# Performance work log

Hardware: AMD Instinct MI355X
Metric: run time of the kernel (lower is better)

The kernel has to match this reference:

```python
import jax, jax.numpy as jnp
import numpy as np

TEMPERATURE = 0.1
EPS_NORM = 1e-12   # F.normalize eps
EPS_DEN = 1e-08


def setup_inputs() -> dict:
    key = jax.random.key(0)
    k1, k2 = jax.random.split(key)
    N, D = 8192, 256
    representations = jax.random.normal(k1, (N, D), dtype=jnp.float32)
    pseudo_labels = jax.random.randint(k2, (N,), 0, 100, dtype=jnp.int64)
    return {"representations": representations, "pseudo_labels": pseudo_labels}


def reference(representations, pseudo_labels):
    N = representations.shape[0]
    # L2 normalize rows (torch F.normalize semantics: x / max(||x||, eps))
    norm = jnp.linalg.norm(representations, axis=1, keepdims=True)
    r = representations / jnp.maximum(norm, EPS_NORM)
    # N x N cosine similarity
    sim = r @ r.T
    same = pseudo_labels[:, None] == pseudo_labels[None, :]
    eye = jnp.eye(N, dtype=bool)
    positive_mask = (same & ~eye).astype(sim.dtype)   # diag removed
    negative_mask = (~same).astype(sim.dtype)
    numerator = jnp.exp(sim * positive_mask / TEMPERATURE)
    num_diag = jnp.diagonal(numerator)                 # = exp(0) = 1 on diag
    denominator = jnp.sum(jnp.exp(sim * negative_mask / TEMPERATURE), axis=1) + num_diag
    loss = jnp.mean(-jnp.log(num_diag / (denominator + EPS_DEN)))
    return loss
```

## Files before the change

kernel.cpp:

```cpp
#include <hip/hip_runtime.h>
#include <hip/hip_bf16.h>
#include <hip/hip_fp8.h>
#include <stdint.h>

typedef __attribute__((ext_vector_type(4))) float f32x4;
typedef __attribute__((ext_vector_type(4))) unsigned int u32x4;
typedef __attribute__((ext_vector_type(8))) int i32x8;

#define N_ROWS 8192
#define DIM 256
#define BM 128
#define BJ 128
#define JCHUNKS 8
#define JCHUNK (N_ROWS / JCHUNKS)

#define SCL 3.79828252f

#define UNIT_SCALE 0x7F7F7F7F

__global__ void k_norm(const float* __restrict__ reps,
                       unsigned char* __restrict__ rq,
                       float* __restrict__ den,
                       float* __restrict__ out) {
  const int w = threadIdx.x >> 6, lane = threadIdx.x & 63;
  const int row = blockIdx.x * 4 + w;
  const float4 v = reinterpret_cast<const float4*>(reps + row * DIM)[lane];
  float ss = v.x * v.x + v.y * v.y + v.z * v.z + v.w * v.w;
#pragma unroll
  for (int m = 1; m < 64; m <<= 1) ss += __shfl_xor(ss, m);
  const float scale = SCL / fmaxf(sqrtf(ss), 1e-12f);
  const uint32_t b0 = __hip_fp8_e4m3(v.x * scale).__x;
  const uint32_t b1 = __hip_fp8_e4m3(v.y * scale).__x;
  const uint32_t b2 = __hip_fp8_e4m3(v.z * scale).__x;
  const uint32_t b3 = __hip_fp8_e4m3(v.w * scale).__x;
  *reinterpret_cast<uint32_t*>(rq + (size_t)row * DIM + lane * 4) =
      b0 | (b1 << 8) | (b2 << 16) | (b3 << 24);
  if (threadIdx.x < 4) den[blockIdx.x * 4 + threadIdx.x] = 0.0f;
  if (blockIdx.x == 0 && threadIdx.x == 0) out[0] = 0.0f;
}

__global__ __launch_bounds__(256, 2) void k_sim(
    const unsigned char* __restrict__ rq,
    const int* __restrict__ lab,
    float* __restrict__ den) {
  __shared__ unsigned char Bs[2][BJ * DIM];

  const int tid = threadIdx.x;
  const int w = tid >> 6, lane = tid & 63;
  const int l15 = lane & 15, lq = lane >> 4;
  const int ibase = blockIdx.x * BM + w * 32;
  const int jc0 = blockIdx.y * JCHUNK;

  i32x8 a[2][2];
#pragma unroll
  for (int t = 0; t < 2; ++t) {
    const unsigned char* ap = rq + (size_t)(ibase + t * 16 + l15) * DIM + lq * 32;
#pragma unroll
    for (int kc = 0; kc < 2; ++kc) {
      const u32x4 v0 = *reinterpret_cast<const u32x4*>(ap + kc * 128);
      const u32x4 v1 = *reinterpret_cast<const u32x4*>(ap + kc * 128 + 16);
      a[t][kc] = (i32x8){(int)v0.x, (int)v0.y, (int)v0.z, (int)v0.w,
                         (int)v1.x, (int)v1.y, (int)v1.z, (int)v1.w};
    }
  }
  int labi[2][4];
#pragma unroll
  for (int t = 0; t < 2; ++t)
#pragma unroll
    for (int r = 0; r < 4; ++r)
      labi[t][r] = lab[ibase + t * 16 + lq * 4 + r];

  f32x4 dsum[2] = {{0.f, 0.f, 0.f, 0.f}, {0.f, 0.f, 0.f, 0.f}};

  const int lrow0 = w * 32;

#pragma unroll
  for (int q = 0; q < 8; ++q) {
    const int lrow = lrow0 + q * 4 + lq;
    const int ch = l15 ^ (lrow & 7);
    const unsigned char* g = rq + (size_t)(jc0 + lrow) * DIM + ch * 16;
    unsigned char* l = Bs[0] + (lrow0 + q * 4) * DIM;
    __builtin_amdgcn_global_load_lds(
        (const __attribute__((address_space(1))) uint32_t*)g,
        (__attribute__((address_space(3))) uint32_t*)l, 16, 0, 0);
  }

  for (int jt = 0; jt < JCHUNK / BJ; ++jt) {
    const int cur = jt & 1;
    const int j0 = jc0 + jt * BJ;

    __syncthreads();

    if (jt < JCHUNK / BJ - 1) {
      const int jn = j0 + BJ;
#pragma unroll
      for (int q = 0; q < 8; ++q) {
        const int lrow = lrow0 + q * 4 + lq;
        const int ch = l15 ^ (lrow & 7);
        const unsigned char* g = rq + (size_t)(jn + lrow) * DIM + ch * 16;
        unsigned char* l = Bs[cur ^ 1] + (lrow0 + q * 4) * DIM;
        __builtin_amdgcn_global_load_lds(
            (const __attribute__((address_space(1))) uint32_t*)g,
            (__attribute__((address_space(3))) uint32_t*)l, 16, 0, 0);
      }
    }

    int labj[8];
#pragma unroll
    for (int s = 0; s < 8; ++s) labj[s] = lab[j0 + s * 16 + l15];

    const unsigned char* Bb = Bs[cur];
#pragma unroll
    for (int s = 0; s < 8; ++s) {
      f32x4 acc0 = {0.f, 0.f, 0.f, 0.f};
      f32x4 acc1 = {0.f, 0.f, 0.f, 0.f};
      const int brow = s * 16 + l15;
      const unsigned char* bp = Bb + brow * DIM;
      const int sw = brow & 7;
#pragma unroll
      for (int kc = 0; kc < 2; ++kc) {
        const int base = kc * 8 + lq * 2;
        const u32x4 b0 = *reinterpret_cast<const u32x4*>(bp + (base ^ sw) * 16);
        const u32x4 b1 = *reinterpret_cast<const u32x4*>(bp + ((base + 1) ^ sw) * 16);
        const i32x8 bb = (i32x8){(int)b0.x, (int)b0.y, (int)b0.z, (int)b0.w,
                                 (int)b1.x, (int)b1.y, (int)b1.z, (int)b1.w};
        acc0 = __builtin_amdgcn_mfma_scale_f32_16x16x128_f8f6f4(
            a[0][kc], bb, acc0, 0, 0, 0, UNIT_SCALE, 0, UNIT_SCALE);
        acc1 = __builtin_amdgcn_mfma_scale_f32_16x16x128_f8f6f4(
            a[1][kc], bb, acc1, 0, 0, 0, UNIT_SCALE, 0, UNIT_SCALE);
      }
#pragma unroll
      for (int r = 0; r < 4; ++r) {
        float e0 = __builtin_amdgcn_exp2f(acc0[r]);
        float e1 = __builtin_amdgcn_exp2f(acc1[r]);
        dsum[0][r] += (labi[0][r] == labj[s]) ? 1.0f : e0;
        dsum[1][r] += (labi[1][r] == labj[s]) ? 1.0f : e1;
      }
    }
  }

#pragma unroll
  for (int t = 0; t < 2; ++t)
#pragma unroll
    for (int r = 0; r < 4; ++r) {
      float v = dsum[t][r];
      v += __shfl_xor(v, 1);
      v += __shfl_xor(v, 2);
      v += __shfl_xor(v, 4);
      v += __shfl_xor(v, 8);
      if (l15 == 0) atomicAdd(&den[ibase + t * 16 + lq * 4 + r], v);
    }
}

__global__ void k_loss(const float* __restrict__ den, float* __restrict__ out) {
  const int idx = blockIdx.x * 256 + threadIdx.x;
  float v = logf(den[idx] + 1.0f + 1e-8f);
#pragma unroll
  for (int m = 1; m < 64; m <<= 1) v += __shfl_xor(v, m);
  __shared__ float sred[4];
  if ((threadIdx.x & 63) == 0) sred[threadIdx.x >> 6] = v;
  __syncthreads();
  if (threadIdx.x == 0)
    atomicAdd(out, (sred[0] + sred[1] + sred[2] + sred[3]) * (1.0f / (float)N_ROWS));
}

extern "C" void kernel_launch(void* const* d_in, const int* in_sizes, int n_in,
                              void* d_out, int out_size, void* d_ws, size_t ws_size,
                              hipStream_t stream) {
  const float* reps = (const float*)d_in[0];
  const int* lab = (const int*)d_in[1];
  float* out = (float*)d_out;
  unsigned char* rq = (unsigned char*)d_ws;
  float* den = (float*)((char*)d_ws + (size_t)N_ROWS * DIM);

  k_norm<<<N_ROWS / 4, 256, 0, stream>>>(reps, rq, den, out);
  k_sim<<<dim3(N_ROWS / BM, JCHUNKS), 256, 0, stream>>>(rq, lab, den);
  k_loss<<<N_ROWS / 256, 256, 0, stream>>>(den, out);
}
```

Measured before the change: 35.35 us.

## Switch similarity tile to 32x32x64 FP8 MFMA with 256-row blocks

Replaces the 16x16x128 scaled FP8 MFMA with the 32x32x64 variant, so each wave computes a 64-row by 32-column tile per step. The block's row tile doubles to 256 and the column split doubles to 16 chunks. Labels are packed into bytes to keep register use down with the larger accumulators. This aims for higher MFMA throughput and more B-tile reuse from LDS, at the cost of more accumulator and exp work per thread and the loss of the occupancy hint.

Result: slower. 52.04 us (+47.2%).

```diff
diff --git a/kernel.cpp b/kernel.cpp
--- a/kernel.cpp
+++ b/kernel.cpp
@@ -4,14 +4,15 @@
 #include <stdint.h>
 
 typedef __attribute__((ext_vector_type(4))) float f32x4;
+typedef __attribute__((ext_vector_type(16))) float f32x16;
 typedef __attribute__((ext_vector_type(4))) unsigned int u32x4;
 typedef __attribute__((ext_vector_type(8))) int i32x8;
 
 #define N_ROWS 8192
 #define DIM 256
-#define BM 128
+#define BM 256
 #define BJ 128
-#define JCHUNKS 8
+#define JCHUNKS 16
 #define JCHUNK (N_ROWS / JCHUNKS)
 
 #define SCL 3.79828252f
@@ -39,7 +40,7 @@
   if (blockIdx.x == 0 && threadIdx.x == 0) out[0] = 0.0f;
 }
 
-__global__ __launch_bounds__(256, 2) void k_sim(
+__global__ __attribute__((amdgpu_flat_work_group_size(256, 256))) void k_sim(
     const unsigned char* __restrict__ rq,
     const int* __restrict__ lab,
     float* __restrict__ den) {
@@ -48,29 +49,40 @@
   const int tid = threadIdx.x;
   const int w = tid >> 6, lane = tid & 63;
   const int l15 = lane & 15, lq = lane >> 4;
-  const int ibase = blockIdx.x * BM + w * 32;
+  const int l31 = lane & 31, lh = lane >> 5;
+  const int ibase = blockIdx.x * BM + w * 64;
   const int jc0 = blockIdx.y * JCHUNK;
 
-  i32x8 a[2][2];
+  i32x8 a[2][4];
 #pragma unroll
   for (int t = 0; t < 2; ++t) {
-    const unsigned char* ap = rq + (size_t)(ibase + t * 16 + l15) * DIM + lq * 32;
+    const unsigned char* ap = rq + (size_t)(ibase + t * 32 + l31) * DIM + lh * 32;
 #pragma unroll
-    for (int kc = 0; kc < 2; ++kc) {
-      const u32x4 v0 = *reinterpret_cast<const u32x4*>(ap + kc * 128);
-      const u32x4 v1 = *reinterpret_cast<const u32x4*>(ap + kc * 128 + 16);
+    for (int kc = 0; kc < 4; ++kc) {
+      const u32x4 v0 = *reinterpret_cast<const u32x4*>(ap + kc * 64);
+      const u32x4 v1 = *reinterpret_cast<const u32x4*>(ap + kc * 64 + 16);
       a[t][kc] = (i32x8){(int)v0.x, (int)v0.y, (int)v0.z, (int)v0.w,
                          (int)v1.x, (int)v1.y, (int)v1.z, (int)v1.w};
     }
   }
-  int labi[2][4];
+
+  uint32_t labi_pk[2][4];
 #pragma unroll
   for (int t = 0; t < 2; ++t)
 #pragma unroll
-    for (int r = 0; r < 4; ++r)
-      labi[t][r] = lab[ibase + t * 16 + lq * 4 + r];
+    for (int g = 0; g < 4; ++g) {
+      const int base = ibase + t * 32 + 8 * g + 4 * lh;
+      labi_pk[t][g] = (uint32_t)(lab[base] & 0xFF) |
+                      ((uint32_t)(lab[base + 1] & 0xFF) << 8) |
+                      ((uint32_t)(lab[base + 2] & 0xFF) << 16) |
+                      ((uint32_t)(lab[base + 3] & 0xFF) << 24);
+    }
 
-  f32x4 dsum[2] = {{0.f, 0.f, 0.f, 0.f}, {0.f, 0.f, 0.f, 0.f}};
+  f32x16 dsum[2];
+#pragma unroll
+  for (int t = 0; t < 2; ++t)
+#pragma unroll
+    for (int r = 0; r < 16; ++r) dsum[t][r] = 0.0f;
 
   const int lrow0 = w * 32;
 
@@ -105,36 +117,42 @@
       }
     }
 
-    int labj[8];
-#pragma unroll
-    for (int s = 0; s < 8; ++s) labj[s] = lab[j0 + s * 16 + l15];
+    const uint32_t labj_pk =
+        (uint32_t)(lab[j0 + l31] & 0xFF) |
+        ((uint32_t)(lab[j0 + 32 + l31] & 0xFF) << 8) |
+        ((uint32_t)(lab[j0 + 64 + l31] & 0xFF) << 16) |
+        ((uint32_t)(lab[j0 + 96 + l31] & 0xFF) << 24);
 
     const unsigned char* Bb = Bs[cur];
 #pragma unroll
-    for (int s = 0; s < 8; ++s) {
-      f32x4 acc0 = {0.f, 0.f, 0.f, 0.f};
-      f32x4 acc1 = {0.f, 0.f, 0.f, 0.f};
-      const int brow = s * 16 + l15;
+    for (int s = 0; s < 4; ++s) {
+      f32x16 acc0, acc1;
+#pragma unroll
+      for (int r = 0; r < 16; ++r) { acc0[r] = 0.0f; acc1[r] = 0.0f; }
+      const int brow = s * 32 + l31;
       const unsigned char* bp = Bb + brow * DIM;
       const int sw = brow & 7;
 #pragma unroll
-      for (int kc = 0; kc < 2; ++kc) {
-        const int base = kc * 8 + lq * 2;
-        const u32x4 b0 = *reinterpret_cast<const u32x4*>(bp + (base ^ sw) * 16);
-        const u32x4 b1 = *reinterpret_cast<const u32x4*>(bp + ((base + 1) ^ sw) * 16);
+      for (int kc = 0; kc < 4; ++kc) {
+        const int c0 = kc * 4 + lh * 2;
+        const u32x4 b0 = *reinterpret_cast<const u32x4*>(bp + (c0 ^ sw) * 16);
+        const u32x4 b1 = *reinterpret_cast<const u32x4*>(bp + ((c0 + 1) ^ sw) * 16);
         const i32x8 bb = (i32x8){(int)b0.x, (int)b0.y, (int)b0.z, (int)b0.w,
                                  (int)b1.x, (int)b1.y, (int)b1.z, (int)b1.w};
-        acc0 = __builtin_amdgcn_mfma_scale_f32_16x16x128_f8f6f4(
+        acc0 = __builtin_amdgcn_mfma_scale_f32_32x32x64_f8f6f4(
             a[0][kc], bb, acc0, 0, 0, 0, UNIT_SCALE, 0, UNIT_SCALE);
-        acc1 = __builtin_amdgcn_mfma_scale_f32_16x16x128_f8f6f4(
+        acc1 = __builtin_amdgcn_mfma_scale_f32_32x32x64_f8f6f4(
             a[1][kc], bb, acc1, 0, 0, 0, UNIT_SCALE, 0, UNIT_SCALE);
       }
+      const int lj = (int)((labj_pk >> (s * 8)) & 0xFF);
 #pragma unroll
-      for (int r = 0; r < 4; ++r) {
-        float e0 = __builtin_amdgcn_exp2f(acc0[r]);
-        float e1 = __builtin_amdgcn_exp2f(acc1[r]);
-        dsum[0][r] += (labi[0][r] == labj[s]) ? 1.0f : e0;
-        dsum[1][r] += (labi[1][r] == labj[s]) ? 1.0f : e1;
+      for (int r = 0; r < 16; ++r) {
+        const float e0 = __builtin_amdgcn_exp2f(acc0[r]);
+        const float e1 = __builtin_amdgcn_exp2f(acc1[r]);
+        const int li0 = (int)((labi_pk[0][r >> 2] >> ((r & 3) * 8)) & 0xFF);
+        const int li1 = (int)((labi_pk[1][r >> 2] >> ((r & 3) * 8)) & 0xFF);
+        dsum[0][r] += (li0 == lj) ? 1.0f : e0;
+        dsum[1][r] += (li1 == lj) ? 1.0f : e1;
       }
     }
   }
@@ -142,13 +160,15 @@
 #pragma unroll
   for (int t = 0; t < 2; ++t)
 #pragma unroll
-    for (int r = 0; r < 4; ++r) {
+    for (int r = 0; r < 16; ++r) {
       float v = dsum[t][r];
       v += __shfl_xor(v, 1);
       v += __shfl_xor(v, 2);
       v += __shfl_xor(v, 4);
       v += __shfl_xor(v, 8);
-      if (l15 == 0) atomicAdd(&den[ibase + t * 16 + lq * 4 + r], v);
+      v += __shfl_xor(v, 16);
+      if (l31 == 0)
+        atomicAdd(&den[ibase + t * 32 + (r & 3) + 8 * (r >> 2) + 4 * lh], v);
     }
 }
 
```

## Exploit similarity symmetry by computing only lower-triangular tiles with column partial sums

Applied to the files above, without the earlier changes.

Each block now processes a balanced set of lower-triangular 128x128 tiles, paired as row p with row 63-p, instead of the full NxN grid. Off-diagonal tiles also produce column sums, which go through shared memory into a per-tile-row partial buffer, so the mirrored tile never has to be computed. The loss kernel then reduces 64 partials per row before the log. This roughly halves the MFMA and exp work. In exchange it adds a per-column cross-wave reduction, extra global writes and reads of an N x 64 partial array, and reloads of the A fragment when a block switches tile rows.

After: 52.01 us. +47.1%, slower.

```diff
diff --git a/kernel.cpp b/kernel.cpp
--- a/kernel.cpp
+++ b/kernel.cpp
@@ -4,23 +4,22 @@
 #include <stdint.h>
 
 typedef __attribute__((ext_vector_type(4))) float f32x4;
+typedef __attribute__((ext_vector_type(2))) unsigned int u32x2;
 typedef __attribute__((ext_vector_type(4))) unsigned int u32x4;
 typedef __attribute__((ext_vector_type(8))) int i32x8;
 
 #define N_ROWS 8192
 #define DIM 256
-#define BM 128
 #define BJ 128
-#define JCHUNKS 8
-#define JCHUNK (N_ROWS / JCHUNKS)
+#define NTILE 64
 
 #define SCL 3.79828252f
-
 #define UNIT_SCALE 0x7F7F7F7F
 
 __global__ void k_norm(const float* __restrict__ reps,
                        unsigned char* __restrict__ rq,
                        float* __restrict__ den,
+                       float* __restrict__ part,
                        float* __restrict__ out) {
   const int w = threadIdx.x >> 6, lane = threadIdx.x & 63;
   const int row = blockIdx.x * 4 + w;
@@ -35,80 +34,121 @@
   const uint32_t b3 = __hip_fp8_e4m3(v.w * scale).__x;
   *reinterpret_cast<uint32_t*>(rq + (size_t)row * DIM + lane * 4) =
       b0 | (b1 << 8) | (b2 << 16) | (b3 << 24);
+  part[blockIdx.x * 256 + threadIdx.x] = 0.0f;
   if (threadIdx.x < 4) den[blockIdx.x * 4 + threadIdx.x] = 0.0f;
   if (blockIdx.x == 0 && threadIdx.x == 0) out[0] = 0.0f;
 }
 
-__global__ __launch_bounds__(256, 2) void k_sim(
+__global__ __launch_bounds__(256, 2) void k_simt(
     const unsigned char* __restrict__ rq,
     const int* __restrict__ lab,
-    float* __restrict__ den) {
+    float* __restrict__ den,
+    float* __restrict__ part) {
   __shared__ unsigned char Bs[2][BJ * DIM];
+  __shared__ float colacc[2][4][128];
+
+  const int p = blockIdx.x >> 4;
+  const int q = blockIdx.x & 15;
+  const int c0 = q * 4 + (q > 0 ? 1 : 0);
+  const int nc = (q == 0) ? 5 : 4;
 
   const int tid = threadIdx.x;
   const int w = tid >> 6, lane = tid & 63;
   const int l15 = lane & 15, lq = lane >> 4;
-  const int ibase = blockIdx.x * BM + w * 32;
-  const int jc0 = blockIdx.y * JCHUNK;
+  const int lrow0 = w * 32;
+
+  {
+    int cc = c0;
+    const int tj = (cc <= p) ? cc : (cc - p - 1);
+#pragma unroll
+    for (int qq = 0; qq < 8; ++qq) {
+      const int lrow = lrow0 + qq * 4 + lq;
+      const int ch = l15 ^ (lrow & 7);
+      const unsigned char* g = rq + (size_t)(tj * 128 + lrow) * DIM + ch * 16;
+      unsigned char* l = Bs[0] + (lrow0 + qq * 4) * DIM;
+      __builtin_amdgcn_global_load_lds(
+          (const __attribute__((address_space(1))) uint32_t*)g,
+          (__attribute__((address_space(3))) uint32_t*)l, 16, 0, 0);
+    }
+  }
 
   i32x8 a[2][2];
-#pragma unroll
-  for (int t = 0; t < 2; ++t) {
-    const unsigned char* ap = rq + (size_t)(ibase + t * 16 + l15) * DIM + lq * 32;
-#pragma unroll
-    for (int kc = 0; kc < 2; ++kc) {
-      const u32x4 v0 = *reinterpret_cast<const u32x4*>(ap + kc * 128);
-      const u32x4 v1 = *reinterpret_cast<const u32x4*>(ap + kc * 128 + 16);
-      a[t][kc] = (i32x8){(int)v0.x, (int)v0.y, (int)v0.z, (int)v0.w,
-                         (int)v1.x, (int)v1.y, (int)v1.z, (int)v1.w};
-    }
-  }
   int labi[2][4];
-#pragma unroll
-  for (int t = 0; t < 2; ++t)
-#pragma unroll
-    for (int r = 0; r < 4; ++r)
-      labi[t][r] = lab[ibase + t * 16 + lq * 4 + r];
-
   f32x4 dsum[2] = {{0.f, 0.f, 0.f, 0.f}, {0.f, 0.f, 0.f, 0.f}};
-
-  const int lrow0 = w * 32;
-
-#pragma unroll
-  for (int q = 0; q < 8; ++q) {
-    const int lrow = lrow0 + q * 4 + lq;
-    const int ch = l15 ^ (lrow & 7);
-    const unsigned char* g = rq + (size_t)(jc0 + lrow) * DIM + ch * 16;
-    unsigned char* l = Bs[0] + (lrow0 + q * 4) * DIM;
-    __builtin_amdgcn_global_load_lds(
-        (const __attribute__((address_space(1))) uint32_t*)g,
-        (__attribute__((address_space(3))) uint32_t*)l, 16, 0, 0);
-  }
-
-  for (int jt = 0; jt < JCHUNK / BJ; ++jt) {
-    const int cur = jt & 1;
-    const int j0 = jc0 + jt * BJ;
+  int cur_ti = -1, cur_ibase = 0;
+  int prev_store = 0, prev_ti = 0, prev_tj = 0;
+
+  for (int idx = 0; idx < nc; ++idx) {
+    const int cc = c0 + idx;
+    const int cur = idx & 1;
+    int ti, tj;
+    if (cc <= p) { ti = p; tj = cc; }
+    else         { ti = 63 - p; tj = cc - p - 1; }
+    const int jbase = tj * 128;
 
     __syncthreads();
 
-    if (jt < JCHUNK / BJ - 1) {
-      const int jn = j0 + BJ;
-#pragma unroll
-      for (int q = 0; q < 8; ++q) {
-        const int lrow = lrow0 + q * 4 + lq;
+    if (idx + 1 < nc) {
+      const int ccn = cc + 1;
+      const int tjn = (ccn <= p) ? ccn : (ccn - p - 1);
+#pragma unroll
+      for (int qq = 0; qq < 8; ++qq) {
+        const int lrow = lrow0 + qq * 4 + lq;
         const int ch = l15 ^ (lrow & 7);
-        const unsigned char* g = rq + (size_t)(jn + lrow) * DIM + ch * 16;
-        unsigned char* l = Bs[cur ^ 1] + (lrow0 + q * 4) * DIM;
+        const unsigned char* g = rq + (size_t)(tjn * 128 + lrow) * DIM + ch * 16;
+        unsigned char* l = Bs[cur ^ 1] + (lrow0 + qq * 4) * DIM;
         __builtin_amdgcn_global_load_lds(
             (const __attribute__((address_space(1))) uint32_t*)g,
             (__attribute__((address_space(3))) uint32_t*)l, 16, 0, 0);
       }
     }
 
+    if (prev_store && tid < 128)
+      part[(size_t)prev_ti * N_ROWS + prev_tj * 128 + tid] =
+          colacc[cur ^ 1][0][tid] + colacc[cur ^ 1][1][tid] +
+          colacc[cur ^ 1][2][tid] + colacc[cur ^ 1][3][tid];
+
+    if (ti != cur_ti) {
+      if (cur_ti >= 0) {
+#pragma unroll
+        for (int t = 0; t < 2; ++t)
+#pragma unroll
+          for (int r = 0; r < 4; ++r) {
+            float v = dsum[t][r];
+            v += __shfl_xor(v, 1);
+            v += __shfl_xor(v, 2);
+            v += __shfl_xor(v, 4);
+            v += __shfl_xor(v, 8);
+            if (l15 == 0) atomicAdd(&den[cur_ibase + t * 16 + lq * 4 + r], v);
+            dsum[t][r] = 0.f;
+          }
+      }
+      cur_ti = ti;
+      cur_ibase = ti * 128 + w * 32;
+#pragma unroll
+      for (int t = 0; t < 2; ++t) {
+        const unsigned char* ap =
+            rq + (size_t)(cur_ibase + t * 16 + l15) * DIM + lq * 32;
+#pragma unroll
+        for (int kc = 0; kc < 2; ++kc) {
+          const u32x4 v0 = *reinterpret_cast<const u32x4*>(ap + kc * 128);
+          const u32x4 v1 = *reinterpret_cast<const u32x4*>(ap + kc * 128 + 16);
+          a[t][kc] = (i32x8){(int)v0.x, (int)v0.y, (int)v0.z, (int)v0.w,
+                             (int)v1.x, (int)v1.y, (int)v1.z, (int)v1.w};
+        }
+      }
+#pragma unroll
+      for (int t = 0; t < 2; ++t)
+#pragma unroll
+        for (int r = 0; r < 4; ++r)
+          labi[t][r] = lab[cur_ibase + t * 16 + lq * 4 + r];
+    }
+
     int labj[8];
 #pragma unroll
-    for (int s = 0; s < 8; ++s) labj[s] = lab[j0 + s * 16 + l15];
-
+    for (int s = 0; s < 8; ++s) labj[s] = lab[jbase + s * 16 + l15];
+
+    const bool offd = (ti != tj);
     const unsigned char* Bb = Bs[cur];
 #pragma unroll
     for (int s = 0; s < 8; ++s) {
@@ -129,16 +169,35 @@
         acc1 = __builtin_amdgcn_mfma_scale_f32_16x16x128_f8f6f4(
             a[1][kc], bb, acc1, 0, 0, 0, UNIT_SCALE, 0, UNIT_SCALE);
       }
+      float colp = 0.f;
 #pragma unroll
       for (int r = 0; r < 4; ++r) {
-        float e0 = __builtin_amdgcn_exp2f(acc0[r]);
-        float e1 = __builtin_amdgcn_exp2f(acc1[r]);
-        dsum[0][r] += (labi[0][r] == labj[s]) ? 1.0f : e0;
-        dsum[1][r] += (labi[1][r] == labj[s]) ? 1.0f : e1;
-      }
-    }
+        const float e0 = __builtin_amdgcn_exp2f(acc0[r]);
+        const float e1 = __builtin_amdgcn_exp2f(acc1[r]);
+        const float m0 = (labi[0][r] == labj[s]) ? 1.0f : e0;
+        const float m1 = (labi[1][r] == labj[s]) ? 1.0f : e1;
+        dsum[0][r] += m0;
+        dsum[1][r] += m1;
+        colp += m0 + m1;
+      }
+      if (offd) {
+        colp += __shfl_xor(colp, 16);
+        colp += __shfl_xor(colp, 32);
+        if (lane < 16) colacc[cur][w][s * 16 + l15] = colp;
+      }
+    }
+    prev_store = offd ? 1 : 0;
+    prev_ti = ti;
+    prev_tj = tj;
   }
 
+  __syncthreads();
+  if (prev_store && tid < 128) {
+    const int lastbuf = (nc - 1) & 1;
+    part[(size_t)prev_ti * N_ROWS + prev_tj * 128 + tid] =
+        colacc[lastbuf][0][tid] + colacc[lastbuf][1][tid] +
+        colacc[lastbuf][2][tid] + colacc[lastbuf][3][tid];
+  }
 #pragma unroll
   for (int t = 0; t < 2; ++t)
 #pragma unroll
@@ -148,13 +207,18 @@
       v += __shfl_xor(v, 2);
       v += __shfl_xor(v, 4);
       v += __shfl_xor(v, 8);
-      if (l15 == 0) atomicAdd(&den[ibase + t * 16 + lq * 4 + r], v);
-    }
-}
-
-__global__ void k_loss(const float* __restrict__ den, float* __restrict__ out) {
+      if (l15 == 0) atomicAdd(&den[cur_ibase + t * 16 + lq * 4 + r], v);
+    }
+}
+
+__global__ void k_loss(const float* __restrict__ den,
+                       const float* __restrict__ part,
+                       float* __restrict__ out) {
   const int idx = blockIdx.x * 256 + threadIdx.x;
-  float v = logf(den[idx] + 1.0f + 1e-8f);
+  float v = den[idx] + 1.0f + 1e-8f;
+#pragma unroll
+  for (int a2 = 0; a2 < NTILE; ++a2) v += part[(size_t)a2 * N_ROWS + idx];
+  v = logf(v);
 #pragma unroll
   for (int m = 1; m < 64; m <<= 1) v += __shfl_xor(v, m);
   __shared__ float sred[4];
@@ -172,8 +236,10 @@
   float* out = (float*)d_out;
   unsigned char* rq = (unsigned char*)d_ws;
   float* den = (float*)((char*)d_ws + (size_t)N_ROWS * DIM);
-
-  k_norm<<<N_ROWS / 4, 256, 0, stream>>>(reps, rq, den, out);
-  k_sim<<<dim3(N_ROWS / BM, JCHUNKS), 256, 0, stream>>>(rq, lab, den);
-  k_loss<<<N_ROWS / 256, 256, 0, stream>>>(den, out);
-}
+  float* part = (float*)((char*)d_ws + (size_t)N_ROWS * DIM
+                         + (size_t)N_ROWS * 4);
+
+  k_norm<<<N_ROWS / 4, 256, 0, stream>>>(reps, rq, den, part, out);
+  k_simt<<<512, 256, 0, stream>>>(rq, lab, den, part);
+  k_loss<<<N_ROWS / 256, 256, 0, stream>>>(den, part, out);
+}
```

## Quantize normalized rows to FP4 e2m1 and use scaled FP4 MFMA

Applied to the files above, without the earlier changes.

Normalized representations are now quantized to 4-bit e2m1 with a custom rounding function instead of fp8 e4m3, halving the stored row size. The similarity kernel loads half as many bytes into LDS and from global memory, and runs the scaled MFMA in fp4 mode with a block scale of 2^-3 to undo the pre-scaling. This cuts memory traffic and may raise MFMA throughput. The cost is a large loss of precision in the cosine similarities, which, after the divide by temperature and the exp, could move the loss far from the fp32 reference.

Result: faster. 30.28 us (-14.4%).

```diff
diff --git a/kernel.cpp b/kernel.cpp
--- a/kernel.cpp
+++ b/kernel.cpp
@@ -1,6 +1,5 @@
 #include <hip/hip_runtime.h>
 #include <hip/hip_bf16.h>
-#include <hip/hip_fp8.h>
 #include <stdint.h>
 
 typedef __attribute__((ext_vector_type(4))) float f32x4;
@@ -9,6 +8,7 @@
 
 #define N_ROWS 8192
 #define DIM 256
+#define ROWB 128
 #define BM 128
 #define BJ 128
 #define JCHUNKS 8
@@ -16,7 +16,16 @@
 
 #define SCL 3.79828252f
 
-#define UNIT_SCALE 0x7F7F7F7F
+#define SCALE_M3 0x7C7C7C7C
+
+__device__ __forceinline__ uint32_t q_e2m1(float y) {
+  const uint32_t s = (__builtin_bit_cast(uint32_t, y) >> 31) << 3;
+  const float a = fabsf(y);
+  const uint32_t c = (a < 0.25f) ? 0u : (a < 0.75f) ? 1u : (a < 1.25f) ? 2u
+                   : (a < 1.75f) ? 3u : (a < 2.5f)  ? 4u : (a < 3.5f)  ? 5u
+                   : (a < 5.0f)  ? 6u : 7u;
+  return s | c;
+}
 
 __global__ void k_norm(const float* __restrict__ reps,
                        unsigned char* __restrict__ rq,
@@ -28,13 +37,11 @@
   float ss = v.x * v.x + v.y * v.y + v.z * v.z + v.w * v.w;
 #pragma unroll
   for (int m = 1; m < 64; m <<= 1) ss += __shfl_xor(ss, m);
-  const float scale = SCL / fmaxf(sqrtf(ss), 1e-12f);
-  const uint32_t b0 = __hip_fp8_e4m3(v.x * scale).__x;
-  const uint32_t b1 = __hip_fp8_e4m3(v.y * scale).__x;
-  const uint32_t b2 = __hip_fp8_e4m3(v.z * scale).__x;
-  const uint32_t b3 = __hip_fp8_e4m3(v.w * scale).__x;
-  *reinterpret_cast<uint32_t*>(rq + (size_t)row * DIM + lane * 4) =
-      b0 | (b1 << 8) | (b2 << 16) | (b3 << 24);
+  const float qs = 8.0f * SCL / fmaxf(sqrtf(ss), 1e-12f);
+  const uint32_t nib = q_e2m1(v.x * qs) | (q_e2m1(v.y * qs) << 4) |
+                       (q_e2m1(v.z * qs) << 8) | (q_e2m1(v.w * qs) << 12);
+  *reinterpret_cast<unsigned short*>(rq + (size_t)row * ROWB + lane * 2) =
+      (unsigned short)nib;
   if (threadIdx.x < 4) den[blockIdx.x * 4 + threadIdx.x] = 0.0f;
   if (blockIdx.x == 0 && threadIdx.x == 0) out[0] = 0.0f;
 }
@@ -43,7 +50,7 @@
     const unsigned char* __restrict__ rq,
     const int* __restrict__ lab,
     float* __restrict__ den) {
-  __shared__ unsigned char Bs[2][BJ * DIM];
+  __shared__ unsigned char Bs[2][BJ * ROWB];
 
   const int tid = threadIdx.x;
   const int w = tid >> 6, lane = tid & 63;
@@ -54,13 +61,11 @@
   i32x8 a[2][2];
 #pragma unroll
   for (int t = 0; t < 2; ++t) {
-    const unsigned char* ap = rq + (size_t)(ibase + t * 16 + l15) * DIM + lq * 32;
+    const unsigned char* ap = rq + (size_t)(ibase + t * 16 + l15) * ROWB;
 #pragma unroll
     for (int kc = 0; kc < 2; ++kc) {
-      const u32x4 v0 = *reinterpret_cast<const u32x4*>(ap + kc * 128);
-      const u32x4 v1 = *reinterpret_cast<const u32x4*>(ap + kc * 128 + 16);
-      a[t][kc] = (i32x8){(int)v0.x, (int)v0.y, (int)v0.z, (int)v0.w,
-                         (int)v1.x, (int)v1.y, (int)v1.z, (int)v1.w};
+      const u32x4 v0 = *reinterpret_cast<const u32x4*>(ap + kc * 64 + lq * 16);
+      a[t][kc] = (i32x8){(int)v0.x, (int)v0.y, (int)v0.z, (int)v0.w, 0, 0, 0, 0};
     }
   }
   int labi[2][4];
@@ -75,11 +80,11 @@
   const int lrow0 = w * 32;
 
 #pragma unroll
-  for (int q = 0; q < 8; ++q) {
-    const int lrow = lrow0 + q * 4 + lq;
-    const int ch = l15 ^ (lrow & 7);
-    const unsigned char* g = rq + (size_t)(jc0 + lrow) * DIM + ch * 16;
-    unsigned char* l = Bs[0] + (lrow0 + q * 4) * DIM;
+  for (int q = 0; q < 4; ++q) {
+    const int lrow = lrow0 + q * 8 + (lane >> 3);
+    const int ch = (lane & 7) ^ (lrow & 7);
+    const unsigned char* g = rq + (size_t)(jc0 + lrow) * ROWB + ch * 16;
+    unsigned char* l = Bs[0] + (lrow0 + q * 8) * ROWB;
     __builtin_amdgcn_global_load_lds(
         (const __attribute__((address_space(1))) uint32_t*)g,
         (__attribute__((address_space(3))) uint32_t*)l, 16, 0, 0);
@@ -94,11 +99,11 @@
     if (jt < JCHUNK / BJ - 1) {
       const int jn = j0 + BJ;
 #pragma unroll
-      for (int q = 0; q < 8; ++q) {
-        const int lrow = lrow0 + q * 4 + lq;
-        const int ch = l15 ^ (lrow & 7);
-        const unsigned char* g = rq + (size_t)(jn + lrow) * DIM + ch * 16;
-        unsigned char* l = Bs[cur ^ 1] + (lrow0 + q * 4) * DIM;
+      for (int q = 0; q < 4; ++q) {
+        const int lrow = lrow0 + q * 8 + (lane >> 3);
+        const int ch = (lane & 7) ^ (lrow & 7);
+        const unsigned char* g = rq + (size_t)(jn + lrow) * ROWB + ch * 16;
+        unsigned char* l = Bs[cur ^ 1] + (lrow0 + q * 8) * ROWB;
         __builtin_amdgcn_global_load_lds(
             (const __attribute__((address_space(1))) uint32_t*)g,
             (__attribute__((address_space(3))) uint32_t*)l, 16, 0, 0);
@@ -115,24 +120,23 @@
       f32x4 acc0 = {0.f, 0.f, 0.f, 0.f};
       f32x4 acc1 = {0.f, 0.f, 0.f, 0.f};
       const int brow = s * 16 + l15;
-      const unsigned char* bp = Bb + brow * DIM;
+      const unsigned char* bp = Bb + brow * ROWB;
       const int sw = brow & 7;
 #pragma unroll
       for (int kc = 0; kc < 2; ++kc) {
-        const int base = kc * 8 + lq * 2;
-        const u32x4 b0 = *reinterpret_cast<const u32x4*>(bp + (base ^ sw) * 16);
-        const u32x4 b1 = *reinterpret_cast<const u32x4*>(bp + ((base + 1) ^ sw) * 16);
-        const i32x8 bb = (i32x8){(int)b0.x, (int)b0.y, (int)b0.z, (int)b0.w,
-                                 (int)b1.x, (int)b1.y, (int)b1.z, (int)b1.w};
+        const int ch = (kc * 4 + lq) ^ sw;
+        const u32x4 bv = *reinterpret_cast<const u32x4*>(bp + ch * 16);
+        const i32x8 bb =
+            (i32x8){(int)bv.x, (int)bv.y, (int)bv.z, (int)bv.w, 0, 0, 0, 0};
         acc0 = __builtin_amdgcn_mfma_scale_f32_16x16x128_f8f6f4(
-            a[0][kc], bb, acc0, 0, 0, 0, UNIT_SCALE, 0, UNIT_SCALE);
+            a[0][kc], bb, acc0, 4, 4, 0, SCALE_M3, 0, SCALE_M3);
         acc1 = __builtin_amdgcn_mfma_scale_f32_16x16x128_f8f6f4(
-            a[1][kc], bb, acc1, 0, 0, 0, UNIT_SCALE, 0, UNIT_SCALE);
+            a[1][kc], bb, acc1, 4, 4, 0, SCALE_M3, 0, SCALE_M3);
       }
 #pragma unroll
       for (int r = 0; r < 4; ++r) {
-        float e0 = __builtin_amdgcn_exp2f(acc0[r]);
-        float e1 = __builtin_amdgcn_exp2f(acc1[r]);
+        const float e0 = __builtin_amdgcn_exp2f(acc0[r]);
+        const float e1 = __builtin_amdgcn_exp2f(acc1[r]);
         dsum[0][r] += (labi[0][r] == labj[s]) ? 1.0f : e0;
         dsum[1][r] += (labi[1][r] == labj[s]) ? 1.0f : e1;
       }
@@ -171,7 +175,7 @@
   const int* lab = (const int*)d_in[1];
   float* out = (float*)d_out;
   unsigned char* rq = (unsigned char*)d_ws;
-  float* den = (float*)((char*)d_ws + (size_t)N_ROWS * DIM);
+  float* den = (float*)((char*)d_ws + (size_t)N_ROWS * ROWB);
 
   k_norm<<<N_ROWS / 4, 256, 0, stream>>>(reps, rq, den, out);
   k_sim<<<dim3(N_ROWS / BM, JCHUNKS), 256, 0, stream>>>(rq, lab, den);
```
